# Kernel tuning notes

Hardware: AMD Instinct MI355X
Metric: run time of the kernel (lower is better)

The kernel has to match this reference:

```python
import jax, jax.numpy as jnp
import numpy as np

EPS_SLOPE = 1e-4
EPS_AVG = 1e-8
MIN_AVG = 1e-6
EPS_SCALE = 1e-3


def _slopes_yk(xk, delta_raw):
    # xk: [D, K] sorted knot x-positions; delta_raw: [D, K-1]
    seg_dx = xk[:, 1:] - xk[:, :-1]                      # [D, K-1]
    slopes = jax.nn.softplus(delta_raw) + EPS_SLOPE       # [D, K-1]
    avg = (slopes * seg_dx).sum(1, keepdims=True) / (seg_dx.sum(1, keepdims=True) + EPS_AVG)
    avg = jnp.maximum(avg, MIN_AVG)
    slopes = slopes / avg
    yk = jnp.concatenate(
        [jnp.zeros((xk.shape[0], 1), dtype=xk.dtype), jnp.cumsum(slopes * seg_dx, axis=1)],
        axis=1,
    )                                                     # [D, K]
    return slopes, yk


def setup_inputs() -> dict:
    key = jax.random.key(0)
    k1, k2, k3, k4, k5 = jax.random.split(key, 5)
    N, D, K = 1_000_000, 64, 32
    x = jax.random.normal(k1, (N, D), dtype=jnp.float32)
    # sorted knots per dim, spanning roughly the data range
    xk = jnp.sort(jax.random.normal(k2, (D, K), dtype=jnp.float32) * 2.0, axis=1)
    delta_raw = jax.random.normal(k3, (D, K - 1), dtype=jnp.float32) * 0.1
    scale_raw = jax.random.normal(k4, (D,), dtype=jnp.float32) * 0.1
    shift = jax.random.normal(k5, (D,), dtype=jnp.float32) * 0.1
    return {"x": x, "xk": xk, "delta_raw": delta_raw, "scale_raw": scale_raw, "shift": shift}


def reference(x, xk, delta_raw, scale_raw, shift):
    # x: [N, D]; xk: [D, K]
    D, K = xk.shape
    slopes, yk = _slopes_yk(xk, delta_raw)
    xT = x.T                                              # [D, N]
    # per-dim binary search (torch.searchsorted default == side='left')
    idx = jax.vmap(lambda knots, vals: jnp.searchsorted(knots, vals))(xk, xT)
    i0 = jnp.clip(idx, 1, K - 1) - 1                      # [D, N]
    x0 = jnp.take_along_axis(xk, i0, axis=1)              # [D, N]
    y0 = jnp.take_along_axis(yk, i0, axis=1)
    m = jnp.take_along_axis(slopes, i0, axis=1)
    y = (y0 + m * (xT - x0)).T                            # [N, D]
    scale = jax.nn.softplus(scale_raw) + EPS_SCALE
    return y * scale + shift
```

## Files before the change

### kernel.cpp

```cpp
#include <hip/hip_runtime.h>
#include <math.h>

#define D 64
#define KNOTS 32
#define NSEG 31
#define G 512
#define TPAD 516
#define SPAD 33

typedef float f4v __attribute__((ext_vector_type(4)));

__device__ __forceinline__ float softplus_f(float v) {
  return fmaxf(v, 0.f) + log1pf(expf(-fabsf(v)));
}

__global__ __launch_bounds__(1024, 8) void pwl_fused(
    const float* __restrict__ x, const float* __restrict__ xk,
    const float* __restrict__ delta_raw, const float* __restrict__ scale_raw,
    const float* __restrict__ shift, float* __restrict__ out, int nrows) {
  __shared__ float kL[KNOTS * D];
  __shared__ float sA[D * SPAD];
  __shared__ float sB[D * SPAD];
  __shared__ unsigned char tab[D * TPAD];
  __shared__ float invS[D], nloS[D];

  const int tid = threadIdx.x;

  for (int i = tid; i < D * KNOTS; i += blockDim.x) {
    int d = i >> 5, j = i & 31;
    int sd = (d >> 2) | ((d & 3) << 4);
    kL[j * D + sd] = xk[i];
  }
  __syncthreads();

  if (tid < D) {
    const int sd = tid;
    const int d = ((sd & 15) << 2) | (sd >> 4);
    float num = 0.f, den = 0.f;
    for (int s = 0; s < NSEG; ++s) {
      float sp = softplus_f(delta_raw[d * NSEG + s]) + 1e-4f;
      float dx = kL[(s + 1) * D + sd] - kL[s * D + sd];
      num += sp * dx;
      den += dx;
    }
    float avg = fmaxf(num / (den + 1e-8f), 1e-6f);
    float scale = softplus_f(scale_raw[d]) + 1e-3f;
    float sh = shift[d];
    float y = 0.f;
    for (int s = 0; s < NSEG; ++s) {
      float sp = softplus_f(delta_raw[d * NSEG + s]) + 1e-4f;
      float m = sp / avg;
      float k0 = kL[s * D + sd];
      sA[sd * SPAD + s] = m * scale;
      sB[sd * SPAD + s] = (y - m * k0) * scale + sh;
      y += m * (kL[(s + 1) * D + sd] - k0);
    }
    float lo = kL[1 * D + sd];
    float hi = kL[(KNOTS - 1) * D + sd];
    float inv = (float)G / (hi - lo);
    invS[sd] = inv;
    nloS[sd] = -lo * inv;
  }
  __syncthreads();

  for (int p = tid; p < G * D; p += blockDim.x) {
    const int sd = p & 63;
    const int c = p >> 6;
    const float inv = invS[sd], nlo = nloS[sd];
    int b = 0;
#pragma unroll
    for (int half = 16; half > 0; half >>= 1) {
      float kv = kL[(b + half) * D + sd];
      float cf = fminf(fmaxf(fmaf(kv, inv, nlo), 0.f), (float)(G - 1));
      b += ((int)cf < c) ? half : 0;
    }
    tab[sd * TPAD + c] = (unsigned char)min(b, 30);
  }
  __syncthreads();

  const int lane = tid & 63;
  const int q = lane & 15;
  const int sd0 = q, sd1 = q + 16, sd2 = q + 32, sd3 = q + 48;
  const float inv0 = invS[sd0], nlo0 = nloS[sd0];
  const float inv1 = invS[sd1], nlo1 = nloS[sd1];
  const float inv2 = invS[sd2], nlo2 = nloS[sd2];
  const float inv3 = invS[sd3], nlo3 = nloS[sd3];

  const f4v* __restrict__ x4 = (const f4v*)x;
  f4v* __restrict__ o4 = (f4v*)out;

  auto evalquad = [&](f4v xv) -> f4v {
    float cf0 = fminf(fmaxf(fmaf(xv.x, inv0, nlo0), 0.f), (float)(G - 1));
    float cf1 = fminf(fmaxf(fmaf(xv.y, inv1, nlo1), 0.f), (float)(G - 1));
    float cf2 = fminf(fmaxf(fmaf(xv.z, inv2, nlo2), 0.f), (float)(G - 1));
    float cf3 = fminf(fmaxf(fmaf(xv.w, inv3, nlo3), 0.f), (float)(G - 1));
    int i0 = tab[sd0 * TPAD + (int)cf0];
    int i1 = tab[sd1 * TPAD + (int)cf1];
    int i2 = tab[sd2 * TPAD + (int)cf2];
    int i3 = tab[sd3 * TPAD + (int)cf3];
    f4v r;
    r.x = fmaf(sA[sd0 * SPAD + i0], xv.x, sB[sd0 * SPAD + i0]);
    r.y = fmaf(sA[sd1 * SPAD + i1], xv.y, sB[sd1 * SPAD + i1]);
    r.z = fmaf(sA[sd2 * SPAD + i2], xv.z, sB[sd2 * SPAD + i2]);
    r.w = fmaf(sA[sd3 * SPAD + i3], xv.w, sB[sd3 * SPAD + i3]);
    return r;
  };

  const int gwave = (int)(blockIdx.x * blockDim.x + tid) >> 6;
  const int nwave = (int)(gridDim.x * blockDim.x) >> 6;
  const int ngroups = nrows >> 3;
  const int chunk = (ngroups + nwave - 1) / nwave;
  int g = gwave * chunk;
  const int gend = min(g + chunk, ngroups);

  f4v a0, a1, b0, b1, c0, c1, d0, d1;

#define LOADG(p, gg)                            \
  {                                             \
    const int base_ = (gg) * 128 + lane;        \
    p##0 = x4[base_];                           \
    p##1 = x4[base_ + 64];                      \
  }

#define PROCG(p, gg)                                                       \
  {                                                                        \
    const int base_ = (gg) * 128 + lane;                                   \
    f4v r_;                                                                \
    r_ = evalquad(p##0); __builtin_nontemporal_store(r_, &o4[base_]);      \
    r_ = evalquad(p##1); __builtin_nontemporal_store(r_, &o4[base_ + 64]); \
  }

  if (g < gend) {
    const int glast = gend - 1;
    int gl = g;
    LOADG(a, gl); gl = min(gl + 1, glast);
    LOADG(b, gl); gl = min(gl + 1, glast);
    LOADG(c, gl); gl = min(gl + 1, glast);
    while (true) {
      LOADG(d, gl); gl = min(gl + 1, glast);
      PROCG(a, g); if (++g == gend) break;
      LOADG(a, gl); gl = min(gl + 1, glast);
      PROCG(b, g); if (++g == gend) break;
      LOADG(b, gl); gl = min(gl + 1, glast);
      PROCG(c, g); if (++g == gend) break;
      LOADG(c, gl); gl = min(gl + 1, glast);
      PROCG(d, g); if (++g == gend) break;
    }
  }
#undef LOADG
#undef PROCG

  const int tr0 = ngroups << 3;
  for (int r = tr0 + gwave; r < nrows; r += nwave) {
    if (lane < 16) {
      const int bi = r * 16 + q;
      f4v xv = x4[bi];
      f4v rv = evalquad(xv);
      __builtin_nontemporal_store(rv, &o4[bi]);
    }
  }
}

extern "C" void kernel_launch(void* const* d_in, const int* in_sizes, int n_in,
                              void* d_out, int out_size, void* d_ws, size_t ws_size,
                              hipStream_t stream) {
  const float* x = (const float*)d_in[0];
  const float* xk = (const float*)d_in[1];
  const float* delta_raw = (const float*)d_in[2];
  const float* scale_raw = (const float*)d_in[3];
  const float* shift = (const float*)d_in[4];
  float* out = (float*)d_out;

  const int nrows = in_sizes[0] / D;
  const int block = 1024;
  const int grid = 512;
  pwl_fused<<<grid, block, 0, stream>>>(x, xk, delta_raw, scale_raw, shift,
                                        out, nrows);
}
```

Before: 114.9 us.

## Hand-schedule streaming loop with inline-asm loads/stores and explicit vmcnt pipelining

Replaces the compiler-scheduled 4-deep group pipeline with a 3-stage software pipeline of 16-row groups. It issues global_load/store_dwordx4 through inline assembly with immediate offsets and uses explicit s_waitcnt vmcnt counts so loads for later groups stay in flight while earlier ones are computed. Block size drops from 1024 to 512 threads with matching launch bounds, which halves the total wave count and gives each wave more work. The hand-tuned waitcnt values are fragile: they depend on the exact ordering of memory ops and on correct address clamping.

New measurement: 125.0 us. +8.8%, slower.

```diff
diff --git a/kernel.cpp b/kernel.cpp
--- a/kernel.cpp
+++ b/kernel.cpp
@@ -14,7 +14,7 @@
   return fmaxf(v, 0.f) + log1pf(expf(-fabsf(v)));
 }
 
-__global__ __launch_bounds__(1024, 8) void pwl_fused(
+__global__ __launch_bounds__(512, 4) void pwl_fused(
     const float* __restrict__ x, const float* __restrict__ xk,
     const float* __restrict__ delta_raw, const float* __restrict__ scale_raw,
     const float* __restrict__ shift, float* __restrict__ out, int nrows) {
@@ -86,6 +86,8 @@
   const float inv2 = invS[sd2], nlo2 = nloS[sd2];
   const float inv3 = invS[sd3], nlo3 = nloS[sd3];
 
+  const float* xp = x;
+  float* op = out;
   const f4v* __restrict__ x4 = (const f4v*)x;
   f4v* __restrict__ o4 = (f4v*)out;
 
@@ -106,52 +108,92 @@
     return r;
   };
 
-  const int gwave = (int)(blockIdx.x * blockDim.x + tid) >> 6;
-  const int nwave = (int)(gridDim.x * blockDim.x) >> 6;
-  const int ngroups = nrows >> 3;
-  const int chunk = (ngroups + nwave - 1) / nwave;
-  int g = gwave * chunk;
-  const int gend = min(g + chunk, ngroups);
-
-  f4v a0, a1, b0, b1, c0, c1, d0, d1;
-
-#define LOADG(p, gg)                            \
-  {                                             \
-    const int base_ = (gg) * 128 + lane;        \
-    p##0 = x4[base_];                           \
-    p##1 = x4[base_ + 64];                      \
-  }
-
-#define PROCG(p, gg)                                                       \
-  {                                                                        \
-    const int base_ = (gg) * 128 + lane;                                   \
-    f4v r_;                                                                \
-    r_ = evalquad(p##0); __builtin_nontemporal_store(r_, &o4[base_]);      \
-    r_ = evalquad(p##1); __builtin_nontemporal_store(r_, &o4[base_ + 64]); \
-  }
-
-  if (g < gend) {
-    const int glast = gend - 1;
-    int gl = g;
-    LOADG(a, gl); gl = min(gl + 1, glast);
-    LOADG(b, gl); gl = min(gl + 1, glast);
-    LOADG(c, gl); gl = min(gl + 1, glast);
-    while (true) {
-      LOADG(d, gl); gl = min(gl + 1, glast);
-      PROCG(a, g); if (++g == gend) break;
-      LOADG(a, gl); gl = min(gl + 1, glast);
-      PROCG(b, g); if (++g == gend) break;
-      LOADG(b, gl); gl = min(gl + 1, glast);
-      PROCG(c, g); if (++g == gend) break;
-      LOADG(c, gl); gl = min(gl + 1, glast);
-      PROCG(d, g); if (++g == gend) break;
-    }
-  }
-#undef LOADG
-#undef PROCG
-
-  const int tr0 = ngroups << 3;
-  for (int r = tr0 + gwave; r < nrows; r += nwave) {
+  const int wid = (int)(blockIdx.x * blockDim.x + tid) >> 6;
+  const int nw = (int)(gridDim.x * blockDim.x) >> 6;
+  const int ngroups = nrows >> 4;
+  const int chunk = (ngroups + nw - 1) / nw;
+  int g0 = wid * chunk;
+  const int gend = min(g0 + chunk, ngroups);
+  const int navail = (gend > g0) ? (gend - g0) : 0;
+  const int nfull = (navail / 3) * 3;
+
+  f4v A0, A1, A2, A3, B0, B1, B2, B3, C0, C1, C2, C3;
+
+#define GLOADI(bk, voff)                                                 \
+  asm volatile("global_load_dwordx4 %0, %4, %5 offset:0\n\t"             \
+               "global_load_dwordx4 %1, %4, %5 offset:1024\n\t"          \
+               "global_load_dwordx4 %2, %4, %5 offset:2048\n\t"          \
+               "global_load_dwordx4 %3, %4, %5 offset:3072"              \
+               : "=&v"(bk##0), "=&v"(bk##1), "=&v"(bk##2), "=&v"(bk##3)  \
+               : "v"(voff), "s"(xp))
+
+#define WAITP(NSTR)                                              \
+  asm volatile("s_waitcnt vmcnt(" NSTR ") expcnt(0)" ::: "memory"); \
+  __builtin_amdgcn_sched_barrier(0)
+
+#define STEP(bk, NSTR)                                                   \
+  {                                                                      \
+    WAITP(NSTR);                                                         \
+    f4v r0_ = evalquad(bk##0);                                           \
+    f4v r1_ = evalquad(bk##1);                                           \
+    f4v r2_ = evalquad(bk##2);                                           \
+    f4v r3_ = evalquad(bk##3);                                           \
+    GLOADI(bk, voffN);                                                   \
+    voffN = min(voffN + 4096u, maxL);                                    \
+    asm volatile("global_store_dwordx4 %4, %0, %5 offset:0 nt\n\t"       \
+                 "global_store_dwordx4 %4, %1, %5 offset:1024 nt\n\t"    \
+                 "global_store_dwordx4 %4, %2, %5 offset:2048 nt\n\t"    \
+                 "global_store_dwordx4 %4, %3, %5 offset:3072 nt"        \
+                 :: "v"(r0_), "v"(r1_), "v"(r2_), "v"(r3_),              \
+                    "v"(voffS), "s"(op));                                \
+    voffS += 4096u;                                                      \
+  }
+
+  if (nfull >= 3) {
+    const unsigned lb = (unsigned)lane * 16u;
+    const unsigned maxL = (unsigned)(ngroups - 1) * 4096u + lb;
+    unsigned voffS = (unsigned)g0 * 4096u + lb;
+    unsigned voffN = voffS;
+    GLOADI(A, voffN); voffN += 4096u;
+    GLOADI(B, voffN); voffN += 4096u;
+    GLOADI(C, voffN);
+    voffN = min(voffN + 4096u, maxL);
+
+    STEP(A, "8");
+    STEP(B, "12");
+    STEP(C, "16");
+    const int trips3 = nfull / 3 - 1;
+    for (int t = 0; t < trips3; ++t) {
+      STEP(A, "20");
+      STEP(B, "20");
+      STEP(C, "20");
+    }
+    asm volatile("s_waitcnt vmcnt(0)" ::: "memory");
+    __builtin_amdgcn_sched_barrier(0);
+    g0 += nfull;
+  }
+#undef GLOADI
+#undef WAITP
+#undef STEP
+
+  for (int g = g0; g < gend; ++g) {
+    const int base = g * 256 + lane;
+    f4v v0 = x4[base];
+    f4v v1 = x4[base + 64];
+    f4v v2 = x4[base + 128];
+    f4v v3 = x4[base + 192];
+    f4v r0 = evalquad(v0);
+    f4v r1 = evalquad(v1);
+    f4v r2 = evalquad(v2);
+    f4v r3 = evalquad(v3);
+    __builtin_nontemporal_store(r0, &o4[base]);
+    __builtin_nontemporal_store(r1, &o4[base + 64]);
+    __builtin_nontemporal_store(r2, &o4[base + 128]);
+    __builtin_nontemporal_store(r3, &o4[base + 192]);
+  }
+
+  const int tr0 = ngroups << 4;
+  for (int r = tr0 + wid; r < nrows; r += nw) {
     if (lane < 16) {
       const int bi = r * 16 + q;
       f4v xv = x4[bi];
@@ -172,7 +214,7 @@
   float* out = (float*)d_out;
 
   const int nrows = in_sizes[0] / D;
-  const int block = 1024;
+  const int block = 512;
   const int grid = 512;
   pwl_fused<<<grid, block, 0, stream>>>(x, xk, delta_raw, scale_raw, shift,
                                         out, nrows);
```
